# Performance work log

Measured on AMD Instinct MI355X. Metric: run time of the kernel, lower is better.

## Reference

```python
import jax, jax.numpy as jnp
import numpy as np

C_T, C_Z, C_HID, N_HEADS = 64, 128, 16, 4
N_TEMPL, N_RES = 4, 512
INF = 1e9


def setup_inputs() -> dict:
    key = jax.random.key(0)
    ks = jax.random.split(key, 7)
    return {
        "t": jax.random.normal(ks[0], (N_TEMPL, N_RES, N_RES, C_T), jnp.float32),
        "z": jax.random.normal(ks[1], (N_RES, N_RES, C_Z), jnp.float32),
        "template_mask": jnp.ones((N_TEMPL,), jnp.float32),
        "wq": jax.random.normal(ks[2], (C_Z, N_HEADS * C_HID), jnp.float32) * 0.05,
        "wk": jax.random.normal(ks[3], (C_T, N_HEADS * C_HID), jnp.float32) * 0.05,
        "wv": jax.random.normal(ks[4], (C_T, N_HEADS * C_HID), jnp.float32) * 0.05,
        "wo": jax.random.normal(ks[5], (N_HEADS * C_HID, C_Z), jnp.float32) * 0.05,
        "bo": jnp.zeros((C_Z,), jnp.float32),
    }


def reference(t, z, template_mask, wq, wk, wv, wo, bo):
    # t: [S, N, N, C_t]  z: [N, N, C_z]  template_mask: [S]
    h, d = N_HEADS, C_HID
    bias = INF * (template_mask - 1.0)  # [S], 0 for kept, -inf for masked
    tp = jnp.transpose(t, (1, 2, 0, 3))  # [N, N, S, C_t] (permute_final_dims (1,2,0,3))
    scale = 1.0 / jnp.sqrt(jnp.asarray(d, z.dtype))
    q = jnp.einsum("ijc,chd->ijhd", z, wq.reshape(C_Z, h, d)) * scale  # [N,N,h,d]
    k = jnp.einsum("ijsc,chd->ijshd", tp, wk.reshape(C_T, h, d))       # [N,N,S,h,d]
    v = jnp.einsum("ijsc,chd->ijshd", tp, wv.reshape(C_T, h, d))
    logits = jnp.einsum("ijhd,ijshd->ijhs", q, k) + bias  # [N,N,h,S]
    a = jax.nn.softmax(logits, axis=-1)
    o = jnp.einsum("ijhs,ijshd->ijhd", a, v).reshape(N_RES, N_RES, h * d)
    out = o @ wo + bo  # [N, N, C_z]
    out = out * (jnp.sum(template_mask) > 0).astype(out.dtype)
    return out
```

## Files before the change

kernel.cpp:

```cpp
#include <hip/hip_runtime.h>

#define NRES 512
#define CZ   128
#define CT   64

typedef short bf16x8 __attribute__((ext_vector_type(8)));
typedef short bf16x4 __attribute__((ext_vector_type(4)));
typedef float f32x4  __attribute__((ext_vector_type(4)));

#define MFMA16(a,b,c) __builtin_amdgcn_mfma_f32_16x16x32_bf16((a),(b),(c),0,0,0)

__device__ __forceinline__ unsigned short f2bf(float f){
  unsigned int u = __builtin_bit_cast(unsigned int, f);
  u += 0x7fffu + ((u >> 16) & 1u);
  return (unsigned short)(u >> 16);
}
__device__ __forceinline__ float bf2f(short b){
  return __builtin_bit_cast(float, ((unsigned int)(unsigned short)b) << 16);
}

__global__ void prep_pack(const float* __restrict__ wq, const float* __restrict__ wk,
                          const float* __restrict__ wv, const float* __restrict__ wo,
                          unsigned short* __restrict__ packed){
  int idx = blockIdx.x * 256 + threadIdx.x;
  if (idx >= 48 * 64) return;
  int f = idx >> 6, lane = idx & 63;
  const float* W; int Ncols, nt, ks; float scale = 1.0f;
  if (f < 16)      { W = wq; Ncols = 64;  nt = f >> 2;        ks = f & 3;        scale = 0.25f; }
  else if (f < 24) { W = wk; Ncols = 64;  nt = (f - 16) >> 1; ks = (f - 16) & 1; }
  else if (f < 32) { W = wv; Ncols = 64;  nt = (f - 24) >> 1; ks = (f - 24) & 1; }
  else             { W = wo; Ncols = 128; nt = (f - 32) >> 1; ks = (f - 32) & 1; }
  int col = nt * 16 + (lane & 15);
  int k0  = ks * 32 + (lane >> 4) * 8;
  unsigned short* dst = packed + (size_t)f * 512 + (size_t)lane * 8;
#pragma unroll
  for (int j = 0; j < 8; ++j)
    dst[j] = f2bf(W[(k0 + j) * Ncols + col] * scale);
}

#define TB_OFF 16384
#define O_OFF  16384
#define U23_OFF 49152

__launch_bounds__(256, 2)
__global__ void tpa_main(const float* __restrict__ t, const float* __restrict__ z,
                         const float* __restrict__ mask, const float* __restrict__ bo,
                         const unsigned short* __restrict__ packed,
                         float* __restrict__ out){
  __shared__ __align__(16) char smem[65536];

  const int tid  = threadIdx.x;
  const int lane = tid & 63;
  const int w    = tid >> 6;
  const int b    = blockIdx.x;
  const int i    = b >> 3;
  const int j0   = (b & 7) << 6;

  {
    const float4* zg = reinterpret_cast<const float4*>(z + ((size_t)i * NRES + j0) * CZ);
#pragma unroll
    for (int it = 0; it < 8; ++it){
      int f4  = tid + it * 256;
      int row = f4 >> 5;
      int fc  = f4 & 31;
      float4 v = zg[f4];
      unsigned int lo = (unsigned int)f2bf(v.x) | ((unsigned int)f2bf(v.y) << 16);
      unsigned int hi = (unsigned int)f2bf(v.z) | ((unsigned int)f2bf(v.w) << 16);
      int addr = row * 256 + ((fc * 8) ^ ((row & 7) << 4));
      *reinterpret_cast<uint2*>(smem + addr) = make_uint2(lo, hi);
    }
  }
  {
#pragma unroll
    for (int it = 0; it < 16; ++it){
      int f4 = tid + it * 256;
      int s  = f4 >> 10;
      int r6 = f4 & 1023;
      int row = r6 >> 4;
      int fc  = r6 & 15;
      const float4* tg = reinterpret_cast<const float4*>(
          t + (((size_t)s * NRES + i) * NRES + j0) * CT);
      float4 v = tg[r6];
      unsigned int lo = (unsigned int)f2bf(v.x) | ((unsigned int)f2bf(v.y) << 16);
      unsigned int hi = (unsigned int)f2bf(v.z) | ((unsigned int)f2bf(v.w) << 16);
      int addr = TB_OFF + s * 8192 + row * 128 + ((fc * 8) ^ ((row & 7) << 4));
      *reinterpret_cast<uint2*>(smem + addr) = make_uint2(lo, hi);
    }
  }
  __syncthreads();

  float m0 = mask[0], m1 = mask[1], m2 = mask[2], m3 = mask[3];
  float msum = m0 + m1 + m2 + m3;
  float bias[4] = {1e9f * (m0 - 1.0f), 1e9f * (m1 - 1.0f),
                   1e9f * (m2 - 1.0f), 1e9f * (m3 - 1.0f)};

  const int arow = (w << 4) + (lane & 15);
  const int ksegb = (lane >> 4) * 16;
#define LOADB(fi) (*reinterpret_cast<const bf16x8*>(packed + (size_t)(fi) * 512 + (size_t)lane * 8))

  f32x4 qf[4];
  {
    bf16x8 za[4];
#pragma unroll
    for (int ks = 0; ks < 4; ++ks){
      int kb = ks * 64 + ksegb;
      za[ks] = *reinterpret_cast<const bf16x8*>(smem + arow * 256 + (kb ^ ((arow & 7) << 4)));
    }
#pragma unroll
    for (int nt = 0; nt < 4; ++nt){
      f32x4 acc = {0.f, 0.f, 0.f, 0.f};
#pragma unroll
      for (int ks = 0; ks < 4; ++ks)
        acc = MFMA16(za[ks], LOADB(nt * 4 + ks), acc);
      qf[nt] = acc;
    }
  }

  f32x4 lg[4][4];
#pragma unroll
  for (int s = 0; s < 4; ++s){
    bf16x8 ta[2];
#pragma unroll
    for (int ks = 0; ks < 2; ++ks){
      int kb = ks * 64 + ksegb;
      ta[ks] = *reinterpret_cast<const bf16x8*>(
          smem + TB_OFF + s * 8192 + arow * 128 + (kb ^ ((arow & 7) << 4)));
    }
#pragma unroll
    for (int nt = 0; nt < 4; ++nt){
      f32x4 acc = {0.f, 0.f, 0.f, 0.f};
      acc = MFMA16(ta[0], LOADB(16 + nt * 2 + 0), acc);
      acc = MFMA16(ta[1], LOADB(16 + nt * 2 + 1), acc);
      f32x4 p = acc * qf[nt];
#pragma unroll
      for (int off = 1; off < 16; off <<= 1){
#pragma unroll
        for (int r = 0; r < 4; ++r) p[r] += __shfl_xor(p[r], off);
      }
      lg[s][nt] = p + bias[s];
    }
  }

#pragma unroll
  for (int nt = 0; nt < 4; ++nt){
    f32x4 mx;
#pragma unroll
    for (int r = 0; r < 4; ++r)
      mx[r] = fmaxf(fmaxf(lg[0][nt][r], lg[1][nt][r]), fmaxf(lg[2][nt][r], lg[3][nt][r]));
    f32x4 sum = {0.f, 0.f, 0.f, 0.f};
#pragma unroll
    for (int s = 0; s < 4; ++s){
#pragma unroll
      for (int r = 0; r < 4; ++r) lg[s][nt][r] = __expf(lg[s][nt][r] - mx[r]);
      sum += lg[s][nt];
    }
    f32x4 inv;
#pragma unroll
    for (int r = 0; r < 4; ++r) inv[r] = 1.0f / sum[r];
#pragma unroll
    for (int s = 0; s < 4; ++s) lg[s][nt] *= inv;
  }

  __syncthreads();

  {
    const int g  = lane >> 4, cl = lane & 15;
    const int cb = cl * 8;
#pragma unroll
    for (int r = 0; r < 4; ++r){
      int row = (w << 4) + (g << 2) + r;
      int swzrow = (row & 7) << 4;
      float tv[4][4];
#pragma unroll
      for (int s = 0; s < 4; ++s){
        bf16x4 tq = *reinterpret_cast<const bf16x4*>(
            smem + TB_OFF + s * 8192 + row * 128 + (cb ^ swzrow));
#pragma unroll
        for (int cc = 0; cc < 4; ++cc) tv[s][cc] = bf2f(tq[cc]);
      }
#pragma unroll
      for (int h = 0; h < 4; ++h){
        unsigned int lo, hi;
        float u0 = lg[0][h][r] * tv[0][0] + lg[1][h][r] * tv[1][0] + lg[2][h][r] * tv[2][0] + lg[3][h][r] * tv[3][0];
        float u1 = lg[0][h][r] * tv[0][1] + lg[1][h][r] * tv[1][1] + lg[2][h][r] * tv[2][1] + lg[3][h][r] * tv[3][1];
        float u2 = lg[0][h][r] * tv[0][2] + lg[1][h][r] * tv[1][2] + lg[2][h][r] * tv[2][2] + lg[3][h][r] * tv[3][2];
        float u3 = lg[0][h][r] * tv[0][3] + lg[1][h][r] * tv[1][3] + lg[2][h][r] * tv[2][3] + lg[3][h][r] * tv[3][3];
        lo = (unsigned int)f2bf(u0) | ((unsigned int)f2bf(u1) << 16);
        hi = (unsigned int)f2bf(u2) | ((unsigned int)f2bf(u3) << 16);
        int ubase = (h < 2) ? h * 8192 : U23_OFF + (h - 2) * 8192;
        *reinterpret_cast<uint2*>(smem + ubase + row * 128 + (cb ^ swzrow)) = make_uint2(lo, hi);
      }
    }
  }
  __syncthreads();

  {
    f32x4 of[4];
#pragma unroll
    for (int h = 0; h < 4; ++h){
      int ubase = (h < 2) ? h * 8192 : U23_OFF + (h - 2) * 8192;
      f32x4 acc = {0.f, 0.f, 0.f, 0.f};
#pragma unroll
      for (int ks = 0; ks < 2; ++ks){
        int kb = ks * 64 + ksegb;
        bf16x8 ua = *reinterpret_cast<const bf16x8*>(
            smem + ubase + arow * 128 + (kb ^ ((arow & 7) << 4)));
        acc = MFMA16(ua, LOADB(24 + h * 2 + ks), acc);
      }
      of[h] = acc;
    }
    const int g = lane >> 4, cl = lane & 15;
#pragma unroll
    for (int h = 0; h < 4; ++h){
#pragma unroll
      for (int r = 0; r < 4; ++r){
        int row = (w << 4) + (g << 2) + r;
        int colb = (h * 16 + cl) * 2;
        *reinterpret_cast<unsigned short*>(
            smem + O_OFF + row * 128 + (colb ^ ((row & 7) << 4))) = f2bf(of[h][r]);
      }
    }
  }
  __syncthreads();

  {
    float gate = (msum > 0.0f) ? 1.0f : 0.0f;
    bf16x8 oa[2];
#pragma unroll
    for (int ks = 0; ks < 2; ++ks){
      int kb = ks * 64 + ksegb;
      oa[ks] = *reinterpret_cast<const bf16x8*>(
          smem + O_OFF + arow * 128 + (kb ^ ((arow & 7) << 4)));
    }
    const int g = lane >> 4, cl = lane & 15;
    float* outg = out + ((size_t)i * NRES + j0) * CZ;
#pragma unroll
    for (int nt = 0; nt < 8; ++nt){
      f32x4 acc = {0.f, 0.f, 0.f, 0.f};
      acc = MFMA16(oa[0], LOADB(32 + nt * 2 + 0), acc);
      acc = MFMA16(oa[1], LOADB(32 + nt * 2 + 1), acc);
      int col = nt * 16 + cl;
      float bov = bo[col];
#pragma unroll
      for (int r = 0; r < 4; ++r){
        int lr = (w << 4) + (g << 2) + r;
        outg[(size_t)lr * CZ + col] = (acc[r] + bov) * gate;
      }
    }
  }
}

extern "C" void kernel_launch(void* const* d_in, const int* in_sizes, int n_in,
                              void* d_out, int out_size, void* d_ws, size_t ws_size,
                              hipStream_t stream) {
  const float* t    = (const float*)d_in[0];
  const float* z    = (const float*)d_in[1];
  const float* mask = (const float*)d_in[2];
  const float* wq   = (const float*)d_in[3];
  const float* wk   = (const float*)d_in[4];
  const float* wv   = (const float*)d_in[5];
  const float* wo   = (const float*)d_in[6];
  const float* bo   = (const float*)d_in[7];
  unsigned short* packed = (unsigned short*)d_ws;

  hipLaunchKernelGGL(prep_pack, dim3(12), dim3(256), 0, stream, wq, wk, wv, wo, packed);
  hipLaunchKernelGGL(tpa_main, dim3(4096), dim3(256), 0, stream,
                     t, z, mask, bo, packed, (float*)d_out);
}
```

Baseline: 131.9 us.

## Load z and t directly into MFMA fragments, drop block-wide LDS staging

Each lane now loads its own rows of z and t from global memory straight into registers and packs them to bf16 MFMA A-fragments, so the block-wide LDS staging of inputs is gone. Attention weights are exchanged through a small per-wave LDS scratch, the weighted sum of t (the V path) is computed in registers, and the output projection goes through a per-wave LDS buffer. All __syncthreads are replaced by per-wave lgkmcnt waits. LDS shrinks from 64KB to 13KB and launch bounds rise to 3 blocks per CU to raise occupancy. The cost is higher register pressure and less coalesced per-lane global loads.

```diff
diff --git a/kernel.cpp b/kernel.cpp
--- a/kernel.cpp
+++ b/kernel.cpp
@@ -5,7 +5,6 @@
 #define CT   64
 
 typedef short bf16x8 __attribute__((ext_vector_type(8)));
-typedef short bf16x4 __attribute__((ext_vector_type(4)));
 typedef float f32x4  __attribute__((ext_vector_type(4)));
 
 #define MFMA16(a,b,c) __builtin_amdgcn_mfma_f32_16x16x32_bf16((a),(b),(c),0,0,0)
@@ -17,6 +16,12 @@
 }
 __device__ __forceinline__ float bf2f(short b){
   return __builtin_bit_cast(float, ((unsigned int)(unsigned short)b) << 16);
+}
+__device__ __forceinline__ bf16x8 pack8(const float4 a, const float4 b){
+  bf16x8 r;
+  r[0]=(short)f2bf(a.x); r[1]=(short)f2bf(a.y); r[2]=(short)f2bf(a.z); r[3]=(short)f2bf(a.w);
+  r[4]=(short)f2bf(b.x); r[5]=(short)f2bf(b.y); r[6]=(short)f2bf(b.z); r[7]=(short)f2bf(b.w);
+  return r;
 }
 
 __global__ void prep_pack(const float* __restrict__ wq, const float* __restrict__ wk,
@@ -38,74 +43,56 @@
     dst[j] = f2bf(W[(k0 + j) * Ncols + col] * scale);
 }
 
-#define TB_OFF 16384
-#define O_OFF  16384
-#define U23_OFF 49152
-
-__launch_bounds__(256, 2)
+__launch_bounds__(256, 3)
 __global__ void tpa_main(const float* __restrict__ t, const float* __restrict__ z,
                          const float* __restrict__ mask, const float* __restrict__ bo,
                          const unsigned short* __restrict__ packed,
                          float* __restrict__ out){
-  __shared__ __align__(16) char smem[65536];
+  __shared__ __align__(16) char smem[13312];
 
   const int tid  = threadIdx.x;
   const int lane = tid & 63;
   const int w    = tid >> 6;
+  const int cl   = lane & 15;
+  const int g    = lane >> 4;
   const int b    = blockIdx.x;
   const int i    = b >> 3;
   const int j0   = (b & 7) << 6;
-
-  {
-    const float4* zg = reinterpret_cast<const float4*>(z + ((size_t)i * NRES + j0) * CZ);
-#pragma unroll
-    for (int it = 0; it < 8; ++it){
-      int f4  = tid + it * 256;
-      int row = f4 >> 5;
-      int fc  = f4 & 31;
-      float4 v = zg[f4];
-      unsigned int lo = (unsigned int)f2bf(v.x) | ((unsigned int)f2bf(v.y) << 16);
-      unsigned int hi = (unsigned int)f2bf(v.z) | ((unsigned int)f2bf(v.w) << 16);
-      int addr = row * 256 + ((fc * 8) ^ ((row & 7) << 4));
-      *reinterpret_cast<uint2*>(smem + addr) = make_uint2(lo, hi);
-    }
-  }
-  {
-#pragma unroll
-    for (int it = 0; it < 16; ++it){
-      int f4 = tid + it * 256;
-      int s  = f4 >> 10;
-      int r6 = f4 & 1023;
-      int row = r6 >> 4;
-      int fc  = r6 & 15;
-      const float4* tg = reinterpret_cast<const float4*>(
-          t + (((size_t)s * NRES + i) * NRES + j0) * CT);
-      float4 v = tg[r6];
-      unsigned int lo = (unsigned int)f2bf(v.x) | ((unsigned int)f2bf(v.y) << 16);
-      unsigned int hi = (unsigned int)f2bf(v.z) | ((unsigned int)f2bf(v.w) << 16);
-      int addr = TB_OFF + s * 8192 + row * 128 + ((fc * 8) ^ ((row & 7) << 4));
-      *reinterpret_cast<uint2*>(smem + addr) = make_uint2(lo, hi);
-    }
-  }
-  __syncthreads();
+  const int grow = j0 + (w << 4) + cl;
+
+  const float4* zp = reinterpret_cast<const float4*>(z + ((size_t)i * NRES + grow) * CZ);
+  float4 zraw[8];
+#pragma unroll
+  for (int ks = 0; ks < 4; ++ks)
+#pragma unroll
+    for (int p = 0; p < 2; ++p)
+      zraw[ks * 2 + p] = zp[ks * 8 + g * 2 + p];
+
+  float4 traw[4][4];
+#pragma unroll
+  for (int s = 0; s < 4; ++s){
+    const float4* tp = reinterpret_cast<const float4*>(
+        t + (((size_t)s * NRES + i) * NRES + grow) * CT);
+#pragma unroll
+    for (int ks = 0; ks < 2; ++ks)
+#pragma unroll
+      for (int p = 0; p < 2; ++p)
+        traw[s][ks * 2 + p] = tp[ks * 8 + g * 2 + p];
+  }
 
   float m0 = mask[0], m1 = mask[1], m2 = mask[2], m3 = mask[3];
   float msum = m0 + m1 + m2 + m3;
   float bias[4] = {1e9f * (m0 - 1.0f), 1e9f * (m1 - 1.0f),
                    1e9f * (m2 - 1.0f), 1e9f * (m3 - 1.0f)};
 
-  const int arow = (w << 4) + (lane & 15);
-  const int ksegb = (lane >> 4) * 16;
 #define LOADB(fi) (*reinterpret_cast<const bf16x8*>(packed + (size_t)(fi) * 512 + (size_t)lane * 8))
 
   f32x4 qf[4];
   {
     bf16x8 za[4];
 #pragma unroll
-    for (int ks = 0; ks < 4; ++ks){
-      int kb = ks * 64 + ksegb;
-      za[ks] = *reinterpret_cast<const bf16x8*>(smem + arow * 256 + (kb ^ ((arow & 7) << 4)));
-    }
+    for (int ks = 0; ks < 4; ++ks)
+      za[ks] = pack8(zraw[ks * 2], zraw[ks * 2 + 1]);
 #pragma unroll
     for (int nt = 0; nt < 4; ++nt){
       f32x4 acc = {0.f, 0.f, 0.f, 0.f};
@@ -116,28 +103,30 @@
     }
   }
 
+  bf16x8 ta[4][2];
+#pragma unroll
+  for (int s = 0; s < 4; ++s)
+#pragma unroll
+    for (int ks = 0; ks < 2; ++ks)
+      ta[s][ks] = pack8(traw[s][ks * 2], traw[s][ks * 2 + 1]);
+
   f32x4 lg[4][4];
 #pragma unroll
   for (int s = 0; s < 4; ++s){
-    bf16x8 ta[2];
-#pragma unroll
-    for (int ks = 0; ks < 2; ++ks){
-      int kb = ks * 64 + ksegb;
-      ta[ks] = *reinterpret_cast<const bf16x8*>(
-          smem + TB_OFF + s * 8192 + arow * 128 + (kb ^ ((arow & 7) << 4)));
-    }
 #pragma unroll
     for (int nt = 0; nt < 4; ++nt){
       f32x4 acc = {0.f, 0.f, 0.f, 0.f};
-      acc = MFMA16(ta[0], LOADB(16 + nt * 2 + 0), acc);
-      acc = MFMA16(ta[1], LOADB(16 + nt * 2 + 1), acc);
+      acc = MFMA16(ta[s][0], LOADB(16 + nt * 2 + 0), acc);
+      acc = MFMA16(ta[s][1], LOADB(16 + nt * 2 + 1), acc);
       f32x4 p = acc * qf[nt];
 #pragma unroll
       for (int off = 1; off < 16; off <<= 1){
 #pragma unroll
         for (int r = 0; r < 4; ++r) p[r] += __shfl_xor(p[r], off);
       }
-      lg[s][nt] = p + bias[s];
+#pragma unroll
+      for (int r = 0; r < 4; ++r) p[r] += bias[s];
+      lg[s][nt] = p;
     }
   }
 
@@ -161,79 +150,59 @@
     for (int s = 0; s < 4; ++s) lg[s][nt] *= inv;
   }
 
-  __syncthreads();
+  float* a_ws = reinterpret_cast<float*>(smem + 8192 + w * 1280);
+#pragma unroll
+  for (int s = 0; s < 4; ++s)
+#pragma unroll
+    for (int h = 0; h < 4; ++h)
+      if (cl == s * 4 + h)
+        *reinterpret_cast<f32x4*>(a_ws + (s * 4 + h) * 20 + (g << 2)) = lg[s][h];
+  asm volatile("s_waitcnt lgkmcnt(0)" ::: "memory");
+
+  float as_[4][4];
+#pragma unroll
+  for (int s = 0; s < 4; ++s)
+#pragma unroll
+    for (int h = 0; h < 4; ++h)
+      as_[s][h] = a_ws[(s * 4 + h) * 20 + cl];
+
+  bf16x8 ua[4][2];
+#pragma unroll
+  for (int h = 0; h < 4; ++h)
+#pragma unroll
+    for (int ks = 0; ks < 2; ++ks){
+      float uu[8];
+#pragma unroll
+      for (int j = 0; j < 8; ++j)
+        uu[j] = as_[0][h] * bf2f(ta[0][ks][j]) + as_[1][h] * bf2f(ta[1][ks][j])
+              + as_[2][h] * bf2f(ta[2][ks][j]) + as_[3][h] * bf2f(ta[3][ks][j]);
+#pragma unroll
+      for (int j = 0; j < 8; ++j) ua[h][ks][j] = (short)f2bf(uu[j]);
+    }
+
+  unsigned short* o_ws = reinterpret_cast<unsigned short*>(smem + w * 2048);
+#pragma unroll
+  for (int h = 0; h < 4; ++h){
+    f32x4 acc = {0.f, 0.f, 0.f, 0.f};
+    acc = MFMA16(ua[h][0], LOADB(24 + h * 2 + 0), acc);
+    acc = MFMA16(ua[h][1], LOADB(24 + h * 2 + 1), acc);
+#pragma unroll
+    for (int r = 0; r < 4; ++r){
+      int row = (g << 2) + r;
+      o_ws[row * 64 + ((h * 16 + cl) ^ ((row & 7) << 3))] = (unsigned short)f2bf(acc[r]);
+    }
+  }
+  asm volatile("s_waitcnt lgkmcnt(0)" ::: "memory");
 
   {
-    const int g  = lane >> 4, cl = lane & 15;
-    const int cb = cl * 8;
-#pragma unroll
-    for (int r = 0; r < 4; ++r){
-      int row = (w << 4) + (g << 2) + r;
-      int swzrow = (row & 7) << 4;
-      float tv[4][4];
-#pragma unroll
-      for (int s = 0; s < 4; ++s){
-        bf16x4 tq = *reinterpret_cast<const bf16x4*>(
-            smem + TB_OFF + s * 8192 + row * 128 + (cb ^ swzrow));
-#pragma unroll
-        for (int cc = 0; cc < 4; ++cc) tv[s][cc] = bf2f(tq[cc]);
-      }
-#pragma unroll
-      for (int h = 0; h < 4; ++h){
-        unsigned int lo, hi;
-        float u0 = lg[0][h][r] * tv[0][0] + lg[1][h][r] * tv[1][0] + lg[2][h][r] * tv[2][0] + lg[3][h][r] * tv[3][0];
-        float u1 = lg[0][h][r] * tv[0][1] + lg[1][h][r] * tv[1][1] + lg[2][h][r] * tv[2][1] + lg[3][h][r] * tv[3][1];
-        float u2 = lg[0][h][r] * tv[0][2] + lg[1][h][r] * tv[1][2] + lg[2][h][r] * tv[2][2] + lg[3][h][r] * tv[3][2];
-        float u3 = lg[0][h][r] * tv[0][3] + lg[1][h][r] * tv[1][3] + lg[2][h][r] * tv[2][3] + lg[3][h][r] * tv[3][3];
-        lo = (unsigned int)f2bf(u0) | ((unsigned int)f2bf(u1) << 16);
-        hi = (unsigned int)f2bf(u2) | ((unsigned int)f2bf(u3) << 16);
-        int ubase = (h < 2) ? h * 8192 : U23_OFF + (h - 2) * 8192;
-        *reinterpret_cast<uint2*>(smem + ubase + row * 128 + (cb ^ swzrow)) = make_uint2(lo, hi);
-      }
-    }
-  }
-  __syncthreads();
-
-  {
-    f32x4 of[4];
-#pragma unroll
-    for (int h = 0; h < 4; ++h){
-      int ubase = (h < 2) ? h * 8192 : U23_OFF + (h - 2) * 8192;
-      f32x4 acc = {0.f, 0.f, 0.f, 0.f};
-#pragma unroll
-      for (int ks = 0; ks < 2; ++ks){
-        int kb = ks * 64 + ksegb;
-        bf16x8 ua = *reinterpret_cast<const bf16x8*>(
-            smem + ubase + arow * 128 + (kb ^ ((arow & 7) << 4)));
-        acc = MFMA16(ua, LOADB(24 + h * 2 + ks), acc);
-      }
-      of[h] = acc;
-    }
-    const int g = lane >> 4, cl = lane & 15;
-#pragma unroll
-    for (int h = 0; h < 4; ++h){
-#pragma unroll
-      for (int r = 0; r < 4; ++r){
-        int row = (w << 4) + (g << 2) + r;
-        int colb = (h * 16 + cl) * 2;
-        *reinterpret_cast<unsigned short*>(
-            smem + O_OFF + row * 128 + (colb ^ ((row & 7) << 4))) = f2bf(of[h][r]);
-      }
-    }
-  }
-  __syncthreads();
-
-  {
+    bf16x8 oa[2];
+#pragma unroll
+    for (int ks = 0; ks < 2; ++ks)
+      oa[ks] = *reinterpret_cast<const bf16x8*>(
+          o_ws + cl * 64 + ((ks * 32 + g * 8) ^ ((cl & 7) << 3)));
+
     float gate = (msum > 0.0f) ? 1.0f : 0.0f;
-    bf16x8 oa[2];
-#pragma unroll
-    for (int ks = 0; ks < 2; ++ks){
-      int kb = ks * 64 + ksegb;
-      oa[ks] = *reinterpret_cast<const bf16x8*>(
-          smem + O_OFF + arow * 128 + (kb ^ ((arow & 7) << 4)));
-    }
-    const int g = lane >> 4, cl = lane & 15;
-    float* outg = out + ((size_t)i * NRES + j0) * CZ;
+    float* outg = out + ((size_t)i * NRES + j0 + (w << 4)) * CZ;
 #pragma unroll
     for (int nt = 0; nt < 8; ++nt){
       f32x4 acc = {0.f, 0.f, 0.f, 0.f};
@@ -242,10 +211,8 @@
       int col = nt * 16 + cl;
       float bov = bo[col];
 #pragma unroll
-      for (int r = 0; r < 4; ++r){
-        int lr = (w << 4) + (g << 2) + r;
-        outg[(size_t)lr * CZ + col] = (acc[r] + bov) * gate;
-      }
+      for (int r = 0; r < 4; ++r)
+        outg[(size_t)((g << 2) + r) * CZ + col] = (acc[r] + bov) * gate;
     }
   }
 }
```

New measurement: 267.4 us. 103% more time.
